# Kernel tuning notes

Measured on AMD Instinct MI355X. Metric: run time of the kernel, lower is better.

Reference implementation:

```python
import jax, jax.numpy as jnp
import numpy as np

B, I, J, C, H = 1, 384, 384, 128, 4
CH = 128          # overall hidden
HD = CH // H      # 32 per head
INF = 1000000000.0
EPS = 1e-5


def setup_inputs() -> dict:
    key = jax.random.key(0)
    ks = jax.random.split(key, 10)
    s = 0.02
    return {
        "x": jax.random.normal(ks[0], (B, I, J, C), dtype=jnp.float32),
        "mask": jnp.ones((B, I, J), dtype=jnp.float32),
        "ln_w": jnp.ones((C,), dtype=jnp.float32),
        "ln_b": jnp.zeros((C,), dtype=jnp.float32),
        "wz": jax.random.normal(ks[1], (C, H), dtype=jnp.float32) * s,
        "bz": jnp.zeros((H,), dtype=jnp.float32),
        "wq": jax.random.normal(ks[2], (C, CH), dtype=jnp.float32) * s,
        "wk": jax.random.normal(ks[3], (C, CH), dtype=jnp.float32) * s,
        "wv": jax.random.normal(ks[4], (C, CH), dtype=jnp.float32) * s,
        "wg": jax.random.normal(ks[5], (C, CH), dtype=jnp.float32) * s,
        "bg": jnp.ones((CH,), dtype=jnp.float32),
        "wo": jax.random.normal(ks[6], (CH, C), dtype=jnp.float32) * s,
        "bo": jnp.zeros((C,), dtype=jnp.float32),
    }


def _layer_norm(x, w, b):
    mu = jnp.mean(x, axis=-1, keepdims=True)
    var = jnp.mean(jnp.square(x - mu), axis=-1, keepdims=True)
    return (x - mu) * jax.lax.rsqrt(var + EPS) * w + b


def reference(x, mask, ln_w, ln_b, wz, bz, wq, wk, wv, wg, bg, wo, bo):
    # starting=True: attention over last row axis J
    x = _layer_norm(x, ln_w, ln_b)                      # [B,I,J,C]
    mask_bias = (INF * (mask - 1.0))[:, :, None, None, :]   # [B,I,1,1,J]
    # triangle bias: linear_z then permute (2,0,1), unsqueeze(-4) -> [B,1,H,I,J]
    tri_bias = jnp.einsum("bijc,ch->bhij", x, wz) + bz[None, :, None, None]
    tri_bias = tri_bias[:, None]                        # [B,1,H,I,J]

    q = jnp.einsum("bijc,cd->bijd", x, wq).reshape(B, I, J, H, HD)
    k = jnp.einsum("bijc,cd->bijd", x, wk).reshape(B, I, J, H, HD)
    v = jnp.einsum("bijc,cd->bijd", x, wv).reshape(B, I, J, H, HD)
    q = q / jnp.sqrt(jnp.float32(HD))

    a = jnp.einsum("biqhd,bikhd->bihqk", q, k)          # [B,I,H,J,J]
    a = a + mask_bias + tri_bias
    a = jax.nn.softmax(a, axis=-1)
    o = jnp.einsum("bihqk,bikhd->biqhd", a, v)          # [B,I,J,H,HD]

    g = jax.nn.sigmoid(jnp.einsum("bijc,cd->bijd", x, wg) + bg)
    o = o.reshape(B, I, J, CH) * g
    return jnp.einsum("bijd,dc->bijc", o, wo) + bo      # [B,I,J,C]
```

## Files before the change

### kernel.cpp

```cpp
#include <hip/hip_runtime.h>
#include <math.h>

#define I_DIM 384
#define C_DIM 128
#define H_NUM 4
#define HD_DIM 32
#define M_DIM (I_DIM*I_DIM)
#define INF_F 1000000000.0f
#define EPS_F 1e-5f
#define QSCALE 0.17677669529663687f
#define LOG2E_F 1.4426950408889634f

typedef __attribute__((ext_vector_type(8))) short short8;
typedef __attribute__((ext_vector_type(4))) float f32x4;
union U4S8 { uint4 u; short8 s; };

__device__ __forceinline__ unsigned short f2bf(float f) {
    unsigned int u = __float_as_uint(f);
    u += 0x7fffu + ((u >> 16) & 1u);
    return (unsigned short)(u >> 16);
}
__device__ __forceinline__ float bf2f(unsigned short h) {
    return __uint_as_float((unsigned int)h << 16);
}
__device__ __forceinline__ unsigned int pk2(float a, float b) {
    return (unsigned int)f2bf(a) | ((unsigned int)f2bf(b) << 16);
}
__device__ __forceinline__ unsigned int cvtpk(float lo, float hi) {
    unsigned int r;
    asm("v_cvt_pk_bf16_f32 %0, %1, %2" : "=v"(r) : "v"(lo), "v"(hi));
    return r;
}

__device__ uint4 wfmt_dev[5*4096];

__device__ __forceinline__ void load_lds16(const uint4* gp, void* lp) {
    __builtin_amdgcn_global_load_lds(
        (const __attribute__((address_space(1))) unsigned int*)gp,
        (__attribute__((address_space(3))) unsigned int*)lp,
        16, 0, 0);
}

__global__ __launch_bounds__(256) void wprep_kernel(
    const float* __restrict__ wq, const float* __restrict__ wk,
    const float* __restrict__ wg, const float* __restrict__ wv,
    const float* __restrict__ wo)
{
    const int tid  = blockIdx.x*256 + threadIdx.x;
    const int l    = tid & 63, tile = tid >> 6;
    const int ks   = tile & 3, nt = (tile >> 2) & 7;
    const int s    = (tile >> 5) & 1, m = tile >> 6;
    const float* W = (m==0)?wq:(m==1)?wk:(m==2)?wg:(m==3)?wv:wo;
    const float scale = (m==0) ? QSCALE*LOG2E_F : 1.f;
    const int n  = nt*16 + (l & 15);
    const int kb = ks*32 + (l >> 4)*8;
    unsigned int hw[4];
    #pragma unroll
    for (int jp = 0; jp < 4; ++jp) {
        unsigned short hs[2];
        #pragma unroll
        for (int e = 0; e < 2; ++e) {
            float v = W[(size_t)(kb + jp*2 + e)*C_DIM + n] * scale;
            unsigned short h = f2bf(v);
            if (s) h = f2bf(v - bf2f(h));
            hs[e] = h;
        }
        hw[jp] = (unsigned int)hs[0] | ((unsigned int)hs[1] << 16);
    }
    wfmt_dev[(size_t)m*4096 + (size_t)((s*8 + nt)*4 + ks)*64 + l] =
        make_uint4(hw[0], hw[1], hw[2], hw[3]);
}

__global__ __launch_bounds__(256, 3) void ln_proj_kernel(
    const float* __restrict__ x,
    const float* __restrict__ lnw, const float* __restrict__ lnb,
    const float* __restrict__ wz,  const float* __restrict__ bz,
    const float* __restrict__ bg,
    float* __restrict__ qo, unsigned short* __restrict__ ko16,
    unsigned int* __restrict__ vto, float* __restrict__ go,
    float* __restrict__ zo)
{
    __shared__ __align__(16) unsigned int xs[4096];
    __shared__ __align__(16) uint4 wbuf4[2048];
    unsigned int* vts = xs;

    const int t    = threadIdx.x;
    const int row0 = blockIdx.x * 64;
    const int w = t >> 6, l = t & 63, n16 = l & 15, quad = l >> 4;

    #pragma unroll
    for (int it = 0; it < 4; ++it) {
        const int tl = w*4 + it;
        const int s = tl >> 3, ntl = (tl >> 2) & 1, ks = tl & 3;
        load_lds16(wfmt_dev + (size_t)((s*8 + ntl)*4 + ks)*64 + l,
                   (char*)wbuf4 + tl*1024);
    }

    float4 xv[8];
    const int r = t >> 2, qt = t & 3, c0 = qt * 32;
    const int sw = (r & 7) << 2;
    {
        const float* xrow = x + (size_t)(row0 + r)*C_DIM + c0;
        float s = 0.f, ss = 0.f;
        #pragma unroll
        for (int i2 = 0; i2 < 8; i2++) {
            xv[i2] = ((const float4*)xrow)[i2];
            s  += xv[i2].x + xv[i2].y + xv[i2].z + xv[i2].w;
            ss += xv[i2].x*xv[i2].x + xv[i2].y*xv[i2].y
                + xv[i2].z*xv[i2].z + xv[i2].w*xv[i2].w;
        }
        s  += __shfl_xor(s, 1);  s  += __shfl_xor(s, 2);
        ss += __shfl_xor(ss, 1); ss += __shfl_xor(ss, 2);
        const float mean = s * (1.f/128.f);
        const float var  = ss * (1.f/128.f) - mean*mean;
        const float rstd = rsqrtf(var + EPS_F);
        const float4* wz4 = (const float4*)wz;
        float4 zacc = make_float4(0.f,0.f,0.f,0.f);
        #pragma unroll
        for (int i2 = 0; i2 < 8; i2++) {
            float4 w4 = ((const float4*)(lnw + c0))[i2];
            float4 b4 = ((const float4*)(lnb + c0))[i2];
            float4 r4;
            r4.x = (xv[i2].x - mean)*rstd*w4.x + b4.x;
            r4.y = (xv[i2].y - mean)*rstd*w4.y + b4.y;
            r4.z = (xv[i2].z - mean)*rstd*w4.z + b4.z;
            r4.w = (xv[i2].w - mean)*rstd*w4.w + b4.w;
            const float4 za = wz4[c0 + i2*4 + 0];
            const float4 zb_ = wz4[c0 + i2*4 + 1];
            const float4 zc = wz4[c0 + i2*4 + 2];
            const float4 zd = wz4[c0 + i2*4 + 3];
            zacc.x += r4.x*za.x + r4.y*zb_.x + r4.z*zc.x + r4.w*zd.x;
            zacc.y += r4.x*za.y + r4.y*zb_.y + r4.z*zc.y + r4.w*zd.y;
            zacc.z += r4.x*za.z + r4.y*zb_.z + r4.z*zc.z + r4.w*zd.z;
            zacc.w += r4.x*za.w + r4.y*zb_.w + r4.z*zc.w + r4.w*zd.w;
            const int wi = r*64 + qt*16 + i2*2;
            xs[(wi  ) ^ sw] = pk2(r4.x, r4.y);
            xs[(wi+1) ^ sw] = pk2(r4.z, r4.w);
            xv[i2] = r4;
        }
        zacc.x += __shfl_xor(zacc.x, 1); zacc.x += __shfl_xor(zacc.x, 2);
        zacc.y += __shfl_xor(zacc.y, 1); zacc.y += __shfl_xor(zacc.y, 2);
        zacc.z += __shfl_xor(zacc.z, 1); zacc.z += __shfl_xor(zacc.z, 2);
        zacc.w += __shfl_xor(zacc.w, 1); zacc.w += __shfl_xor(zacc.w, 2);
        const float zv = (qt==0)?zacc.x:(qt==1)?zacc.y:(qt==2)?zacc.z:zacc.w;
        zo[(size_t)qt*M_DIM + row0 + r] = (zv + bz[qt]) * LOG2E_F;
    }
    __syncthreads();

    U4S8 ah[4], al[4];
    const int arow = w*16 + n16;
    #pragma unroll
    for (int ks = 0; ks < 4; ++ks) {
        const int bofs = arow*256 + ((ks*64 + quad*16) ^ ((arow & 7) << 4));
        ah[ks].u = *(const uint4*)((const char*)xs + bofs);
    }
    __syncthreads();

    #pragma unroll
    for (int i2 = 0; i2 < 8; i2++) {
        const float4 r4 = xv[i2];
        const unsigned short h0 = f2bf(r4.x), h1 = f2bf(r4.y),
                             h2 = f2bf(r4.z), h3 = f2bf(r4.w);
        const int wi = r*64 + qt*16 + i2*2;
        xs[(wi  ) ^ sw] = (unsigned int)f2bf(r4.x - bf2f(h0))
                        | ((unsigned int)f2bf(r4.y - bf2f(h1)) << 16);
        xs[(wi+1) ^ sw] = (unsigned int)f2bf(r4.z - bf2f(h2))
                        | ((unsigned int)f2bf(r4.w - bf2f(h3)) << 16);
    }
    __syncthreads();
    #pragma unroll
    for (int ks = 0; ks < 4; ++ks) {
        const int bofs = arow*256 + ((ks*64 + quad*16) ^ ((arow & 7) << 4));
        al[ks].u = *(const uint4*)((const char*)xs + bofs);
    }

    const int i_blk = row0 / I_DIM;
    const int jp0   = (row0 % I_DIM) >> 1;
    const int rw0   = row0 + w*16 + quad*4;

    int p = 0;
    #pragma unroll
    for (int rd = 0; rd < 16; ++rd) {
        const int mi = rd >> 2, qq = rd & 3;

        if (rd < 15) {
            const int m2 = (rd+1) >> 2, q2 = (rd+1) & 3;
            #pragma unroll
            for (int it = 0; it < 4; ++it) {
                const int tl = w*4 + it;
                const int s = tl >> 3, ntl2 = (tl >> 2) & 1, ks = tl & 3;
                load_lds16(wfmt_dev + (size_t)m2*4096
                           + (size_t)((s*8 + (q2*2 + ntl2))*4 + ks)*64 + l,
                           (char*)wbuf4 + (p^1)*16384 + tl*1024);
            }
        }

        f32x4 acc[2];
        #pragma unroll
        for (int ntl = 0; ntl < 2; ++ntl) {
            f32x4 a = {0.f, 0.f, 0.f, 0.f};
            #pragma unroll
            for (int ks = 0; ks < 4; ++ks) {
                U4S8 bh, bl;
                bh.u = wbuf4[p*1024 + (    ntl*4 + ks)*64 + l];
                bl.u = wbuf4[p*1024 + (8 + ntl*4 + ks)*64 + l];
                a = __builtin_amdgcn_mfma_f32_16x16x32_bf16(ah[ks].s, bh.s, a, 0,0,0);
                a = __builtin_amdgcn_mfma_f32_16x16x32_bf16(al[ks].s, bh.s, a, 0,0,0);
                a = __builtin_amdgcn_mfma_f32_16x16x32_bf16(ah[ks].s, bl.s, a, 0,0,0);
            }
            acc[ntl] = a;
        }

        if (mi == 0) {
            #pragma unroll
            for (int ntl = 0; ntl < 2; ++ntl)
                #pragma unroll
                for (int rr = 0; rr < 4; ++rr)
                    qo[(size_t)(rw0 + rr)*C_DIM + qq*32 + ntl*16 + n16] =
                        acc[ntl][rr];
        } else if (mi == 1) {
            #pragma unroll
            for (int ntl = 0; ntl < 2; ++ntl)
                #pragma unroll
                for (int rr = 0; rr < 4; ++rr)
                    ko16[(size_t)(rw0 + rr)*C_DIM + qq*32 + ntl*16 + n16] =
                        f2bf(acc[ntl][rr]);
        } else if (mi == 2) {
            #pragma unroll
            for (int ntl = 0; ntl < 2; ++ntl) {
                const float bgv = bg[qq*32 + ntl*16 + n16];
                #pragma unroll
                for (int rr = 0; rr < 4; ++rr)
                    go[(size_t)(rw0 + rr)*C_DIM + qq*32 + ntl*16 + n16] =
                        1.f/(1.f + __expf(-(acc[ntl][rr] + bgv)));
            }
        } else {
            #pragma unroll
            for (int ntl = 0; ntl < 2; ++ntl)
                #pragma unroll
                for (int pr = 0; pr < 2; ++pr)
                    vts[(ntl*16 + n16)*33 + w*8 + quad*2 + pr] =
                        pk2(acc[ntl][2*pr], acc[ntl][2*pr+1]);
            __syncthreads();
            for (int idx = t; idx < 32*32; idx += 256) {
                const int ch_l = idx >> 5, pp = idx & 31;
                vto[((size_t)i_blk*C_DIM + qq*32 + ch_l)*192 + jp0 + pp] =
                    vts[ch_l*33 + pp];
            }
        }

        __syncthreads();
        p ^= 1;
    }
}

__global__ __launch_bounds__(256, 3) void attn_mfma_kernel(
    const float* q, const unsigned short* __restrict__ k16,
    const unsigned int* __restrict__ vt32, const float* __restrict__ zb,
    const float* __restrict__ mask, float* o)
{
    __shared__ uint4 Ks4[384*4];
    __shared__ uint4 VTl[32*49];
    __shared__ __align__(16) float mbl[384];

    const int ii = blockIdx.x;
    const int h  = blockIdx.y;
    const int t  = threadIdx.x;
    const size_t rbase = (size_t)ii*I_DIM*C_DIM + h*HD_DIM;

    for (int idx = t; idx < 1536; idx += 256) {
        const int j = idx >> 2, c4 = idx & 3;
        Ks4[j*4 + (c4 ^ ((j >> 1) & 3))] =
            ((const uint4*)k16)[rbase/8 + (size_t)j*16 + c4];
    }
    for (int idx = t; idx < 1536; idx += 256) {
        const int d = idx / 48, m = idx - d*48;
        VTl[d*49 + m] = ((const uint4*)vt32)[((size_t)ii*C_DIM + h*HD_DIM + d)*48 + m];
    }
    for (int jj = t; jj < 384; jj += 256)
        mbl[jj] = (INF_F*LOG2E_F) * (mask[(size_t)ii*I_DIM + jj] - 1.f);
    __syncthreads();

    const int w = t >> 6, l = t & 63;
    const int n16 = l & 15, quad = l >> 4;
    const int slA = n16 + ((quad & 1) << 5);
    const int slB = slA + 16;
    const bool hi = (quad & 2) != 0;

    #pragma unroll 1
    for (int qt = 0; qt < 6; qt++) {
        const int qg = w*6 + qt;

        U4S8 a;
        {
            const float* qrow = q + rbase + (size_t)(qg*16 + n16)*C_DIM + quad*8;
            const float4 f0 = ((const float4*)qrow)[0];
            const float4 f1 = ((const float4*)qrow)[1];
            a.u = make_uint4(cvtpk(f0.x,f0.y), cvtpk(f0.z,f0.w),
                             cvtpk(f1.x,f1.y), cvtpk(f1.z,f1.w));
        }

        f32x4 oacc0 = {0.f,0.f,0.f,0.f}, oacc1 = {0.f,0.f,0.f,0.f};
        float lsum = 0.f;
        const float* zrow = zb + (size_t)h*M_DIM
                          + (size_t)(qg*16 + n16)*I_DIM + quad*4;

        #pragma unroll 2
        for (int c = 0; c < 4; c++) {
            f32x4 cin[6];
            #pragma unroll
            for (int k6 = 0; k6 < 6; k6++) {
                const float4 z4 = *(const float4*)&zrow[96*c + k6*16];
                const float4 m4 = *(const float4*)&mbl[96*c + k6*16 + quad*4];
                cin[k6][0] = z4.x + m4.x;
                cin[k6][1] = z4.y + m4.y;
                cin[k6][2] = z4.z + m4.z;
                cin[k6][3] = z4.w + m4.w;
            }

            f32x4 accS[6];
            __builtin_amdgcn_s_setprio(1);
            #pragma unroll
            for (int k6 = 0; k6 < 6; k6++) {
                const int key = (6*c + k6)*16 + n16;
                U4S8 b;
                b.u = Ks4[key*4 + (quad ^ ((key >> 1) & 3))];
                accS[k6] = __builtin_amdgcn_mfma_f32_16x16x32_bf16(
                    b.s, a.s, cin[k6], 0, 0, 0);
            }
            __builtin_amdgcn_s_setprio(0);

            unsigned int pu[6][2];
            #pragma unroll
            for (int k6 = 0; k6 < 6; k6++) {
                const float e0 = __builtin_amdgcn_exp2f(accS[k6][0]);
                const float e1 = __builtin_amdgcn_exp2f(accS[k6][1]);
                const float e2 = __builtin_amdgcn_exp2f(accS[k6][2]);
                const float e3 = __builtin_amdgcn_exp2f(accS[k6][3]);
                lsum += (e0 + e1) + (e2 + e3);
                pu[k6][0] = cvtpk(e0, e1);
                pu[k6][1] = cvtpk(e2, e3);
            }

            #pragma unroll
            for (int km = 0; km < 3; km++) {
                const unsigned int x0 = __shfl((int)pu[2*km  ][0], slA);
                const unsigned int x1 = __shfl((int)pu[2*km+1][0], slA);
                const unsigned int y0 = __shfl((int)pu[2*km  ][1], slA);
                const unsigned int y1 = __shfl((int)pu[2*km+1][1], slA);
                const unsigned int z0 = __shfl((int)pu[2*km  ][0], slB);
                const unsigned int z1 = __shfl((int)pu[2*km+1][0], slB);
                const unsigned int w0 = __shfl((int)pu[2*km  ][1], slB);
                const unsigned int w1 = __shfl((int)pu[2*km+1][1], slB);
                U4S8 pa;
                pa.u = make_uint4(hi?x1:x0, hi?y1:y0, hi?z1:z0, hi?w1:w0);
                U4S8 vb0, vb1;
                vb0.u = VTl[(n16     )*49 + quad + 4*km + 12*c];
                vb1.u = VTl[(16 + n16)*49 + quad + 4*km + 12*c];
                __builtin_amdgcn_s_setprio(1);
                oacc0 = __builtin_amdgcn_mfma_f32_16x16x32_bf16(vb0.s, pa.s, oacc0, 0,0,0);
                oacc1 = __builtin_amdgcn_mfma_f32_16x16x32_bf16(vb1.s, pa.s, oacc1, 0,0,0);
                __builtin_amdgcn_s_setprio(0);
            }
        }

        float s_ = lsum;
        s_ += __shfl_xor(s_, 16);
        s_ += __shfl_xor(s_, 32);
        const float rcp = 1.f / s_;
        const size_t orow = rbase + (size_t)(qg*16 + n16)*C_DIM;
        float4 o0 = make_float4(oacc0[0]*rcp, oacc0[1]*rcp,
                                oacc0[2]*rcp, oacc0[3]*rcp);
        float4 o1 = make_float4(oacc1[0]*rcp, oacc1[1]*rcp,
                                oacc1[2]*rcp, oacc1[3]*rcp);
        *(float4*)&o[orow + quad*4]      = o0;
        *(float4*)&o[orow + 16 + quad*4] = o1;
    }
}

__global__ __launch_bounds__(256, 3) void out_proj_kernel(
    const float* __restrict__ o, const float* g,
    const float* __restrict__ bo, float* out)
{
    __shared__ __align__(16) unsigned int xs[4096];
    __shared__ __align__(16) uint4 wbuf4[2048];
    const int t    = threadIdx.x;
    const int row0 = blockIdx.x * 64;
    const int w = t >> 6, l = t & 63, n16 = l & 15, quad = l >> 4;

    #pragma unroll
    for (int it = 0; it < 4; ++it) {
        const int tl = w*4 + it;
        const int s = tl >> 3, ntl = (tl >> 2) & 1, ks = tl & 3;
        load_lds16(wfmt_dev + (size_t)4*4096 + (size_t)((s*8 + ntl)*4 + ks)*64 + l,
                   (char*)wbuf4 + tl*1024);
    }

    float4 pv[8];
    const int r = t >> 2, qt = t & 3, c0 = qt * 32;
    const int sw = (r & 7) << 2;
    {
        const float4* orow = (const float4*)(o + (size_t)(row0 + r)*C_DIM + c0);
        const float4* grow = (const float4*)(g + (size_t)(row0 + r)*C_DIM + c0);
        #pragma unroll
        for (int i2 = 0; i2 < 8; i2++) {
            const float4 a = orow[i2];
            const float4 b = grow[i2];
            float4 p;
            p.x = a.x*b.x; p.y = a.y*b.y; p.z = a.z*b.z; p.w = a.w*b.w;
            const int wi = r*64 + qt*16 + i2*2;
            xs[(wi  ) ^ sw] = pk2(p.x, p.y);
            xs[(wi+1) ^ sw] = pk2(p.z, p.w);
            pv[i2] = p;
        }
    }
    __syncthreads();

    U4S8 ah[4], al[4];
    const int arow = w*16 + n16;
    #pragma unroll
    for (int ks = 0; ks < 4; ++ks) {
        const int bofs = arow*256 + ((ks*64 + quad*16) ^ ((arow & 7) << 4));
        ah[ks].u = *(const uint4*)((const char*)xs + bofs);
    }
    __syncthreads();
    #pragma unroll
    for (int i2 = 0; i2 < 8; i2++) {
        const float4 p = pv[i2];
        const unsigned short h0 = f2bf(p.x), h1 = f2bf(p.y),
                             h2 = f2bf(p.z), h3 = f2bf(p.w);
        const int wi = r*64 + qt*16 + i2*2;
        xs[(wi  ) ^ sw] = (unsigned int)f2bf(p.x - bf2f(h0))
                        | ((unsigned int)f2bf(p.y - bf2f(h1)) << 16);
        xs[(wi+1) ^ sw] = (unsigned int)f2bf(p.z - bf2f(h2))
                        | ((unsigned int)f2bf(p.w - bf2f(h3)) << 16);
    }
    __syncthreads();
    #pragma unroll
    for (int ks = 0; ks < 4; ++ks) {
        const int bofs = arow*256 + ((ks*64 + quad*16) ^ ((arow & 7) << 4));
        al[ks].u = *(const uint4*)((const char*)xs + bofs);
    }

    const int rw0 = row0 + w*16 + quad*4;
    int p = 0;
    #pragma unroll
    for (int qq = 0; qq < 4; ++qq) {
        if (qq < 3) {
            const int q2 = qq + 1;
            #pragma unroll
            for (int it = 0; it < 4; ++it) {
                const int tl = w*4 + it;
                const int s = tl >> 3, ntl2 = (tl >> 2) & 1, ks = tl & 3;
                load_lds16(wfmt_dev + (size_t)4*4096
                           + (size_t)((s*8 + (q2*2 + ntl2))*4 + ks)*64 + l,
                           (char*)wbuf4 + (p^1)*16384 + tl*1024);
            }
        }
        f32x4 acc[2];
        #pragma unroll
        for (int ntl = 0; ntl < 2; ++ntl) {
            f32x4 a = {0.f, 0.f, 0.f, 0.f};
            #pragma unroll
            for (int ks = 0; ks < 4; ++ks) {
                U4S8 bh, bl;
                bh.u = wbuf4[p*1024 + (    ntl*4 + ks)*64 + l];
                bl.u = wbuf4[p*1024 + (8 + ntl*4 + ks)*64 + l];
                a = __builtin_amdgcn_mfma_f32_16x16x32_bf16(ah[ks].s, bh.s, a, 0,0,0);
                a = __builtin_amdgcn_mfma_f32_16x16x32_bf16(al[ks].s, bh.s, a, 0,0,0);
                a = __builtin_amdgcn_mfma_f32_16x16x32_bf16(ah[ks].s, bl.s, a, 0,0,0);
            }
            acc[ntl] = a;
        }
        #pragma unroll
        for (int ntl = 0; ntl < 2; ++ntl) {
            const int n = qq*32 + ntl*16 + n16;
            const float bov = bo[n];
            #pragma unroll
            for (int rr = 0; rr < 4; ++rr)
                out[(size_t)(rw0 + rr)*C_DIM + n] = acc[ntl][rr] + bov;
        }
        __syncthreads();
        p ^= 1;
    }
}

extern "C" void kernel_launch(void* const* d_in, const int* in_sizes, int n_in,
                              void* d_out, int out_size, void* d_ws, size_t ws_size,
                              hipStream_t stream)
{
    (void)in_sizes; (void)n_in; (void)out_size; (void)ws_size;
    const float* x    = (const float*)d_in[0];
    const float* mask = (const float*)d_in[1];
    const float* lnw  = (const float*)d_in[2];
    const float* lnb  = (const float*)d_in[3];
    const float* wz   = (const float*)d_in[4];
    const float* bz   = (const float*)d_in[5];
    const float* wq   = (const float*)d_in[6];
    const float* wk   = (const float*)d_in[7];
    const float* wv   = (const float*)d_in[8];
    const float* wg   = (const float*)d_in[9];
    const float* bg   = (const float*)d_in[10];
    const float* wo   = (const float*)d_in[11];
    const float* bo   = (const float*)d_in[12];

    float* ws = (float*)d_ws;
    float* qb   = ws;
    float* zbuf = qb + (size_t)M_DIM*C_DIM;
    unsigned short* kb16 = (unsigned short*)(zbuf + (size_t)H_NUM*M_DIM);
    unsigned int*   vt32 = (unsigned int*)(kb16 + (size_t)M_DIM*C_DIM);
    float* gbuf = (float*)d_out;

    wprep_kernel<<<80, 256, 0, stream>>>(wq, wk, wg, wv, wo);
    ln_proj_kernel<<<M_DIM/64, 256, 0, stream>>>(
        x, lnw, lnb, wz, bz, bg, qb, kb16, vt32, gbuf, zbuf);
    attn_mfma_kernel<<<dim3(I_DIM, H_NUM), 256, 0, stream>>>(
        qb, kb16, vt32, zbuf, mask, qb );
    out_proj_kernel<<<M_DIM/64, 256, 0, stream>>>(
        qb, gbuf, bo, (float*)d_out);
}
```

Before: 435.9 us.

## Store Q as bf16 and fuse gating plus hi/lo split into attention epilogue

The projection kernel now writes Q in bf16 rather than fp32, which halves Q traffic and removes the conversion inside the attention kernel. The attention epilogue reads the gate, multiplies it into the normalized output, and stores a packed bf16 hi/lo pair per element into the output buffer, which has the same size as fp32. The out-projection kernel then reads that single buffer instead of separate o and g buffers and skips its own split arithmetic. The attention kernel takes on a little extra epilogue work, and g and og alias the same output buffer, whose rows are read and then overwritten within the same thread.

```diff
diff --git a/kernel.cpp b/kernel.cpp
--- a/kernel.cpp
+++ b/kernel.cpp
@@ -30,6 +30,11 @@
     unsigned int r;
     asm("v_cvt_pk_bf16_f32 %0, %1, %2" : "=v"(r) : "v"(lo), "v"(hi));
     return r;
+}
+__device__ __forceinline__ unsigned int hl32(float v) {
+    const unsigned short h = f2bf(v);
+    const unsigned short lo = f2bf(v - bf2f(h));
+    return (unsigned int)h | ((unsigned int)lo << 16);
 }
 
 __device__ uint4 wfmt_dev[5*4096];
@@ -76,7 +81,7 @@
     const float* __restrict__ lnw, const float* __restrict__ lnb,
     const float* __restrict__ wz,  const float* __restrict__ bz,
     const float* __restrict__ bg,
-    float* __restrict__ qo, unsigned short* __restrict__ ko16,
+    unsigned short* __restrict__ qo16, unsigned short* __restrict__ ko16,
     unsigned int* __restrict__ vto, float* __restrict__ go,
     float* __restrict__ zo)
 {
@@ -216,8 +221,8 @@
             for (int ntl = 0; ntl < 2; ++ntl)
                 #pragma unroll
                 for (int rr = 0; rr < 4; ++rr)
-                    qo[(size_t)(rw0 + rr)*C_DIM + qq*32 + ntl*16 + n16] =
-                        acc[ntl][rr];
+                    qo16[(size_t)(rw0 + rr)*C_DIM + qq*32 + ntl*16 + n16] =
+                        f2bf(acc[ntl][rr]);
         } else if (mi == 1) {
             #pragma unroll
             for (int ntl = 0; ntl < 2; ++ntl)
@@ -255,9 +260,9 @@
 }
 
 __global__ __launch_bounds__(256, 3) void attn_mfma_kernel(
-    const float* q, const unsigned short* __restrict__ k16,
+    const unsigned short* __restrict__ q16, const unsigned short* __restrict__ k16,
     const unsigned int* __restrict__ vt32, const float* __restrict__ zb,
-    const float* __restrict__ mask, float* o)
+    const float* __restrict__ mask, const float* g, unsigned int* og)
 {
     __shared__ uint4 Ks4[384*4];
     __shared__ uint4 VTl[32*49];
@@ -292,13 +297,7 @@
         const int qg = w*6 + qt;
 
         U4S8 a;
-        {
-            const float* qrow = q + rbase + (size_t)(qg*16 + n16)*C_DIM + quad*8;
-            const float4 f0 = ((const float4*)qrow)[0];
-            const float4 f1 = ((const float4*)qrow)[1];
-            a.u = make_uint4(cvtpk(f0.x,f0.y), cvtpk(f0.z,f0.w),
-                             cvtpk(f1.x,f1.y), cvtpk(f1.z,f1.w));
-        }
+        a.u = *(const uint4*)(q16 + rbase + (size_t)(qg*16 + n16)*C_DIM + quad*8);
 
         f32x4 oacc0 = {0.f,0.f,0.f,0.f}, oacc1 = {0.f,0.f,0.f,0.f};
         float lsum = 0.f;
@@ -369,17 +368,24 @@
         s_ += __shfl_xor(s_, 32);
         const float rcp = 1.f / s_;
         const size_t orow = rbase + (size_t)(qg*16 + n16)*C_DIM;
-        float4 o0 = make_float4(oacc0[0]*rcp, oacc0[1]*rcp,
-                                oacc0[2]*rcp, oacc0[3]*rcp);
-        float4 o1 = make_float4(oacc1[0]*rcp, oacc1[1]*rcp,
-                                oacc1[2]*rcp, oacc1[3]*rcp);
-        *(float4*)&o[orow + quad*4]      = o0;
-        *(float4*)&o[orow + 16 + quad*4] = o1;
+        const float4 g0 = *(const float4*)&g[orow + quad*4];
+        const float4 g1 = *(const float4*)&g[orow + 16 + quad*4];
+        const float o00 = oacc0[0]*rcp, o01 = oacc0[1]*rcp,
+                    o02 = oacc0[2]*rcp, o03 = oacc0[3]*rcp;
+        const float o10 = oacc1[0]*rcp, o11 = oacc1[1]*rcp,
+                    o12 = oacc1[2]*rcp, o13 = oacc1[3]*rcp;
+        uint4 w0_, w1_;
+        w0_.x = hl32(o00*g0.x); w0_.y = hl32(o01*g0.y);
+        w0_.z = hl32(o02*g0.z); w0_.w = hl32(o03*g0.w);
+        w1_.x = hl32(o10*g1.x); w1_.y = hl32(o11*g1.y);
+        w1_.z = hl32(o12*g1.z); w1_.w = hl32(o13*g1.w);
+        *(uint4*)&og[orow + quad*4]      = w0_;
+        *(uint4*)&og[orow + 16 + quad*4] = w1_;
     }
 }
 
 __global__ __launch_bounds__(256, 3) void out_proj_kernel(
-    const float* __restrict__ o, const float* g,
+    const unsigned int* __restrict__ og,
     const float* __restrict__ bo, float* out)
 {
     __shared__ __align__(16) unsigned int xs[4096];
@@ -396,22 +402,17 @@
                    (char*)wbuf4 + tl*1024);
     }
 
-    float4 pv[8];
+    uint4 pw[8];
     const int r = t >> 2, qt = t & 3, c0 = qt * 32;
     const int sw = (r & 7) << 2;
     {
-        const float4* orow = (const float4*)(o + (size_t)(row0 + r)*C_DIM + c0);
-        const float4* grow = (const float4*)(g + (size_t)(row0 + r)*C_DIM + c0);
+        const uint4* prow = (const uint4*)(og + (size_t)(row0 + r)*C_DIM + c0);
         #pragma unroll
         for (int i2 = 0; i2 < 8; i2++) {
-            const float4 a = orow[i2];
-            const float4 b = grow[i2];
-            float4 p;
-            p.x = a.x*b.x; p.y = a.y*b.y; p.z = a.z*b.z; p.w = a.w*b.w;
+            pw[i2] = prow[i2];
             const int wi = r*64 + qt*16 + i2*2;
-            xs[(wi  ) ^ sw] = pk2(p.x, p.y);
-            xs[(wi+1) ^ sw] = pk2(p.z, p.w);
-            pv[i2] = p;
+            xs[(wi  ) ^ sw] = (pw[i2].x & 0xffffu) | (pw[i2].y << 16);
+            xs[(wi+1) ^ sw] = (pw[i2].z & 0xffffu) | (pw[i2].w << 16);
         }
     }
     __syncthreads();
@@ -426,14 +427,9 @@
     __syncthreads();
     #pragma unroll
     for (int i2 = 0; i2 < 8; i2++) {
-        const float4 p = pv[i2];
-        const unsigned short h0 = f2bf(p.x), h1 = f2bf(p.y),
-                             h2 = f2bf(p.z), h3 = f2bf(p.w);
         const int wi = r*64 + qt*16 + i2*2;
-        xs[(wi  ) ^ sw] = (unsigned int)f2bf(p.x - bf2f(h0))
-                        | ((unsigned int)f2bf(p.y - bf2f(h1)) << 16);
-        xs[(wi+1) ^ sw] = (unsigned int)f2bf(p.z - bf2f(h2))
-                        | ((unsigned int)f2bf(p.w - bf2f(h3)) << 16);
+        xs[(wi  ) ^ sw] = (pw[i2].x >> 16) | (pw[i2].y & 0xffff0000u);
+        xs[(wi+1) ^ sw] = (pw[i2].z >> 16) | (pw[i2].w & 0xffff0000u);
     }
     __syncthreads();
     #pragma unroll
@@ -509,13 +505,14 @@
     float* zbuf = qb + (size_t)M_DIM*C_DIM;
     unsigned short* kb16 = (unsigned short*)(zbuf + (size_t)H_NUM*M_DIM);
     unsigned int*   vt32 = (unsigned int*)(kb16 + (size_t)M_DIM*C_DIM);
+    unsigned short* q16  = (unsigned short*)qb;
     float* gbuf = (float*)d_out;
 
     wprep_kernel<<<80, 256, 0, stream>>>(wq, wk, wg, wv, wo);
     ln_proj_kernel<<<M_DIM/64, 256, 0, stream>>>(
-        x, lnw, lnb, wz, bz, bg, qb, kb16, vt32, gbuf, zbuf);
+        x, lnw, lnb, wz, bz, bg, q16, kb16, vt32, gbuf, zbuf);
     attn_mfma_kernel<<<dim3(I_DIM, H_NUM), 256, 0, stream>>>(
-        qb, kb16, vt32, zbuf, mask, qb );
+        q16, kb16, vt32, zbuf, mask, gbuf, (unsigned int*)d_out);
     out_proj_kernel<<<M_DIM/64, 256, 0, stream>>>(
-        qb, gbuf, bo, (float*)d_out);
-}
+        (const unsigned int*)d_out, bo, (float*)d_out);
+}
```

Measured after the change: 416.4 us. -4.5%, faster.
